# Kernel tuning notes

Hardware: AMD Instinct MI355X
Metric: run time of the kernel (lower is better)

## Reference

```python
import jax, jax.numpy as jnp
import numpy as np

B, S, E, H = 16, 2048, 512, 64


def setup_inputs() -> dict:
    key = jax.random.key(0)
    k1, k2, k3, k4, k5 = jax.random.split(key, 5)
    inp = {
        "input": jax.random.normal(k1, (B, S, E), dtype=jnp.float32),
        "seq_lengths": jax.random.randint(k2, (B,), 0, S).astype(jnp.int64),
        "Wq": jax.random.normal(k3, (E, H), dtype=jnp.float32) * (1.0 / np.sqrt(E)),
        "Wk": jax.random.normal(k4, (E, H), dtype=jnp.float32) * (1.0 / np.sqrt(E)),
        "Wv": jax.random.normal(k5, (E, H), dtype=jnp.float32) * (1.0 / np.sqrt(E)),
    }
    return inp


def reference(input, seq_lengths, Wq, Wk, Wv):
    # Projections (bias-free Linear): [B,S,E] @ [E,H] -> [B,S,H]
    q = input @ Wq
    k = input @ Wk
    v = input @ Wv
    Sdim = input.shape[1]
    head_size = Wk.shape[-1]
    # Padding mask: position >= seq_length -> True. Zero out q and k (NOT v),
    # exactly as the torch module does with masked_fill.
    pad = (jnp.arange(Sdim)[None, :] >= seq_lengths[:, None])[:, :, None]  # [B,S,1]
    q = jnp.where(pad, 0.0, q)
    k = jnp.where(pad, 0.0, k)
    scale = 1.0 / np.sqrt(head_size).astype(np.float32)
    # Full score matrix [B,S,S] (the memory-bound intermediate)
    scores = jnp.einsum("bsh,bth->bst", q, k) * scale
    weights = jax.nn.softmax(scores, axis=-1)
    weights = jnp.where(jnp.isnan(weights), 0.0, weights)
    out = jnp.einsum("bst,bth->bsh", weights, v)  # [B,S,H]
    return out
```

## Files before the change

kernel.cpp:

```cpp
#include <hip/hip_runtime.h>
#include <hip/hip_bf16.h>

typedef __bf16 bf16;
typedef __bf16 bf16x8 __attribute__((ext_vector_type(8)));
typedef __bf16 bf16x4 __attribute__((ext_vector_type(4)));
typedef float  f32x4  __attribute__((ext_vector_type(4)));

static constexpr int SDIM = 2048;
static constexpr int EDIM = 512;
static constexpr int HDIM = 64;

typedef __attribute__((address_space(1))) const void* gptr_t;
typedef __attribute__((address_space(3))) void*       lptr_t;

__device__ __forceinline__ void gl_lds16(const bf16* g, bf16* l) {
  __builtin_amdgcn_global_load_lds((gptr_t)g, (lptr_t)l, 16, 0, 0);
}

#if __has_builtin(__builtin_amdgcn_exp2f)
#define EXP2F(x) __builtin_amdgcn_exp2f(x)
#else
#define EXP2F(x) exp2f(x)
#endif

__device__ __forceinline__ bf16x8 pack8(f32x4 a, f32x4 b) {
  bf16x8 r;
  r[0] = (bf16)a[0]; r[1] = (bf16)a[1]; r[2] = (bf16)a[2]; r[3] = (bf16)a[3];
  r[4] = (bf16)b[0]; r[5] = (bf16)b[1]; r[6] = (bf16)b[2]; r[7] = (bf16)b[3];
  return r;
}

__global__ __launch_bounds__(256) void wt_kernel(const float* __restrict__ Wq,
                                                 const float* __restrict__ Wk,
                                                 const float* __restrict__ Wv,
                                                 bf16* __restrict__ Wt) {
  __shared__ float lds[64][65];
  const int mat = blockIdx.x >> 3;
  const int et  = blockIdx.x & 7;
  const float* W = (mat == 0) ? Wq : ((mat == 1) ? Wk : Wv);
  const float scale = (mat == 0) ? 0.18033688f : 1.0f;
  const int t  = threadIdx.x;
  const int er = t >> 2;
  const int c4 = (t & 3) * 16;
#pragma unroll
  for (int j = 0; j < 4; ++j) {
    f32x4 v = *(const f32x4*)(W + (size_t)(et * 64 + er) * HDIM + c4 + j * 4);
    lds[er][c4 + j * 4 + 0] = v[0]; lds[er][c4 + j * 4 + 1] = v[1];
    lds[er][c4 + j * 4 + 2] = v[2]; lds[er][c4 + j * 4 + 3] = v[3];
  }
  __syncthreads();
  const int h  = t >> 2;
  const int ec = (t & 3) * 16;
  bf16x8 o0, o1;
#pragma unroll
  for (int j = 0; j < 8; ++j) o0[j] = (bf16)(lds[ec + j][h] * scale);
#pragma unroll
  for (int j = 0; j < 8; ++j) o1[j] = (bf16)(lds[ec + 8 + j][h] * scale);
  bf16* dst = Wt + mat * (HDIM * EDIM) + (size_t)h * EDIM + et * 64 + ec;
  *(bf16x8*)dst = o0;
  *(bf16x8*)(dst + 8) = o1;
}

__global__ __launch_bounds__(256) void proj_kernel(const float* __restrict__ x,
                                                   const bf16* __restrict__ Wt,
                                                   const int* __restrict__ lens,
                                                   bf16* __restrict__ qo,
                                                   bf16* __restrict__ ko,
                                                   bf16* __restrict__ vT) {
  __shared__ __align__(16) bf16 wbuf[2][192 * 64];
  const int tid  = threadIdx.x;
  const int wave = tid >> 6;
  const int lane = tid & 63;
  const int quad = lane >> 4;
  const int l16  = lane & 15;
  const int rowbase = blockIdx.x * 64 + wave * 16;
  const int b = blockIdx.x >> 5;
  const float* xrow = x + (size_t)(rowbase + l16) * EDIM + quad * 8;
  const int srow   = lane >> 3;
  const int schunk = (lane & 7) ^ srow;

  #define WSTAGE(ck, buf) { _Pragma("unroll")                                  \
    for (int i6 = 0; i6 < 6; ++i6) {                                           \
      const int R0 = (wave * 6 + i6) * 8;                                      \
      gl_lds16(Wt + (size_t)(R0 + srow) * EDIM + (ck) * 64 + schunk * 8,       \
               &(buf)[R0 * 64]); } }

  f32x4 acc[3][4];
#pragma unroll
  for (int m = 0; m < 3; ++m)
#pragma unroll
    for (int nt = 0; nt < 4; ++nt) acc[m][nt] = (f32x4){0.f, 0.f, 0.f, 0.f};

  #define WCOMPUTE(buf, eo4, afrag) { _Pragma("unroll")                        \
    for (int m = 0; m < 3; ++m) { _Pragma("unroll")                            \
      for (int nt = 0; nt < 4; ++nt) {                                         \
        bf16x8 bfv = *(const bf16x8*)(&(buf)[(m * 64 + nt * 16 + l16) * 64 +   \
                                             ((((eo4) + quad) ^ (l16 & 7)) * 8)]); \
        acc[m][nt] = __builtin_amdgcn_mfma_f32_16x16x32_bf16(afrag, bfv, acc[m][nt], 0, 0, 0); } } }

  WSTAGE(0, wbuf[0]);
  f32x4 xA0 = *(const f32x4*)(xrow);
  f32x4 xB0 = *(const f32x4*)(xrow + 4);
  f32x4 xA1 = *(const f32x4*)(xrow + 32);
  f32x4 xB1 = *(const f32x4*)(xrow + 36);
#pragma unroll 2
  for (int ck = 0; ck < 8; ++ck) {
    __syncthreads();
    const int ksn = (ck < 7) ? (ck + 1) * 2 : 14;
    f32x4 nA0 = *(const f32x4*)(xrow + ksn * 32);
    f32x4 nB0 = *(const f32x4*)(xrow + ksn * 32 + 4);
    f32x4 nA1 = *(const f32x4*)(xrow + ksn * 32 + 32);
    f32x4 nB1 = *(const f32x4*)(xrow + ksn * 32 + 36);
    if (ck + 1 < 8) WSTAGE(ck + 1, wbuf[(ck + 1) & 1]);
    bf16x8 a = pack8(xA0, xB0);
    WCOMPUTE(wbuf[ck & 1], 0, a);
    a = pack8(xA1, xB1);
    WCOMPUTE(wbuf[ck & 1], 4, a);
    xA0 = nA0; xB0 = nB0; xA1 = nA1; xB1 = nB1;
  }

  int odd_or = 0;
#pragma unroll
  for (int i = 1; i < 16; i += 2) odd_or |= lens[i];
  const int len = (odd_or == 0) ? lens[2 * b] : lens[b];

#pragma unroll
  for (int nt = 0; nt < 4; ++nt) {
    const int h = nt * 16 + l16;
    bf16x4 vv;
#pragma unroll
    for (int r = 0; r < 4; ++r) {
      const int row = rowbase + quad * 4 + r;
      const int s = row & (SDIM - 1);
      const bool pad = (s >= len);
      qo[(size_t)row * HDIM + h] = (bf16)(pad ? 0.f : acc[0][nt][r]);
      ko[(size_t)row * HDIM + h] = (bf16)(pad ? 0.f : acc[1][nt][r]);
      vv[r] = (bf16)acc[2][nt][r];
    }
    *(bf16x4*)(vT + ((size_t)b * HDIM + h) * SDIM + (rowbase & (SDIM - 1)) + quad * 4) = vv;
  }
  #undef WSTAGE
  #undef WCOMPUTE
}

__global__ __launch_bounds__(256) void attn_kernel(const bf16* __restrict__ qb,
                                                   const bf16* __restrict__ kb,
                                                   const bf16* __restrict__ vT,
                                                   float* __restrict__ out) {
  __shared__ __align__(16) bf16 Kbuf[2][64 * 64];
  __shared__ __align__(16) bf16 Vbuf[2][64 * 64];
  __shared__ __align__(16) bf16 plds[4][2][16 * 64];
  const int tid  = threadIdx.x;
  const int wave = tid >> 6;
  const int lane = tid & 63;
  const int quad = lane >> 4;
  const int l16  = lane & 15;
  const int xcd = blockIdx.x & 7;
  const int jj  = blockIdx.x >> 3;
  const int b   = xcd * 2 + (jj >> 5);
  const int qbase = (jj & 31) * 64 + wave * 16;
  const bf16* q0 = qb + (size_t)b * SDIM * HDIM;
  const bf16* k0 = kb + (size_t)b * SDIM * HDIM;
  const bf16* v0 = vT + (size_t)b * HDIM * SDIM;
  const int swz = (l16 & 7) << 3;
  const int srow   = lane >> 3;
  const int schunk = (lane & 7) ^ (srow & 7);

  bf16x8 qf[2];
#pragma unroll
  for (int c = 0; c < 2; ++c)
    qf[c] = *(const bf16x8*)(q0 + (size_t)(qbase + l16) * HDIM + c * 32 + quad * 8);

  f32x4 O[4];
  float l_acc = 0.f;
#pragma unroll
  for (int ht = 0; ht < 4; ++ht) O[ht] = (f32x4){0.f, 0.f, 0.f, 0.f};
  bf16x8 vfp[4][2];

  #define STAGE(sidx, KB, VB)                                                  \
    {                                                                          \
      const int key0_ = (sidx) * 64;                                           \
      _Pragma("unroll")                                                        \
      for (int j8 = 0; j8 < 2; ++j8) {                                         \
        const int r0 = wave * 16 + j8 * 8;                                     \
        gl_lds16(k0 + (size_t)(key0_ + r0 + srow) * HDIM + schunk * 8,         \
                 &(KB)[r0 * 64]);                                              \
        gl_lds16(v0 + (size_t)(r0 + srow) * SDIM + key0_ + schunk * 8,         \
                 &(VB)[r0 * 64]);                                              \
      }                                                                        \
    }

  STAGE(0, Kbuf[0], Vbuf[0]);
#pragma unroll 2
  for (int s = 0; s < 32; ++s) {
    __syncthreads();
    if (s + 1 < 32) STAGE(s + 1, Kbuf[(s + 1) & 1], Vbuf[(s + 1) & 1]);
    const bf16* KB = Kbuf[s & 1];
    const bf16* VB = Vbuf[s & 1];
    bf16* PW = &plds[wave][s & 1][0];
    const bf16* PR = &plds[wave][(s & 1) ^ 1][0];

    bf16x8 pa[2];
    if (s) {
#pragma unroll
      for (int kc = 0; kc < 2; ++kc)
        pa[kc] = *(const bf16x8*)(&PR[l16 * 64 + (((kc * 4 + quad) << 3) ^ swz)]);
    }

    bf16x8 kf[4][2], vf[4][2];
#pragma unroll
    for (int kt = 0; kt < 4; ++kt)
#pragma unroll
      for (int c = 0; c < 2; ++c)
        kf[kt][c] = *(const bf16x8*)(&KB[(kt * 16 + l16) * 64 + (((c * 4 + quad) << 3) ^ swz)]);
#pragma unroll
    for (int ht = 0; ht < 4; ++ht)
#pragma unroll
      for (int kc = 0; kc < 2; ++kc)
        vf[ht][kc] = *(const bf16x8*)(&VB[(ht * 16 + l16) * 64 + (((kc * 4 + quad) << 3) ^ swz)]);

#pragma unroll
    for (int kt = 0; kt < 4; ++kt) {
      f32x4 st = (f32x4){0.f, 0.f, 0.f, 0.f};
      st = __builtin_amdgcn_mfma_f32_16x16x32_bf16(kf[kt][0], qf[0], st, 0, 0, 0);
      st = __builtin_amdgcn_mfma_f32_16x16x32_bf16(kf[kt][1], qf[1], st, 0, 0, 0);
      f32x4 p;
      p[0] = EXP2F(st[0]); p[1] = EXP2F(st[1]);
      p[2] = EXP2F(st[2]); p[3] = EXP2F(st[3]);
      l_acc += (p[0] + p[1]) + (p[2] + p[3]);
      bf16x4 pb;
      pb[0] = (bf16)p[0]; pb[1] = (bf16)p[1]; pb[2] = (bf16)p[2]; pb[3] = (bf16)p[3];
      const int coff = (((kt * 2 + (quad >> 1)) << 3) ^ swz) + (quad & 1) * 4;
      *(bf16x4*)(&PW[l16 * 64 + coff]) = pb;
    }

    if (s) {
#pragma unroll
      for (int ht = 0; ht < 4; ++ht) {
        O[ht] = __builtin_amdgcn_mfma_f32_16x16x32_bf16(pa[0], vfp[ht][0], O[ht], 0, 0, 0);
        O[ht] = __builtin_amdgcn_mfma_f32_16x16x32_bf16(pa[1], vfp[ht][1], O[ht], 0, 0, 0);
      }
    }
#pragma unroll
    for (int ht = 0; ht < 4; ++ht)
#pragma unroll
      for (int kc = 0; kc < 2; ++kc) vfp[ht][kc] = vf[ht][kc];
  }

  {
    bf16x8 pa[2];
    const bf16* PR = &plds[wave][1][0];
#pragma unroll
    for (int kc = 0; kc < 2; ++kc)
      pa[kc] = *(const bf16x8*)(&PR[l16 * 64 + (((kc * 4 + quad) << 3) ^ swz)]);
#pragma unroll
    for (int ht = 0; ht < 4; ++ht) {
      O[ht] = __builtin_amdgcn_mfma_f32_16x16x32_bf16(pa[0], vfp[ht][0], O[ht], 0, 0, 0);
      O[ht] = __builtin_amdgcn_mfma_f32_16x16x32_bf16(pa[1], vfp[ht][1], O[ht], 0, 0, 0);
    }
  }

  l_acc += __shfl_xor(l_acc, 16);
  l_acc += __shfl_xor(l_acc, 32);
  const float inv_own = 1.0f / l_acc;
#pragma unroll
  for (int r = 0; r < 4; ++r) {
    const float inv = __shfl(inv_own, (lane & 48) + quad * 4 + r);
    const int row = qbase + quad * 4 + r;
#pragma unroll
    for (int ht = 0; ht < 4; ++ht)
      out[((size_t)b * SDIM + row) * HDIM + ht * 16 + l16] = O[ht][r] * inv;
  }
  #undef STAGE
}

extern "C" void kernel_launch(void* const* d_in, const int* in_sizes, int n_in,
                              void* d_out, int out_size, void* d_ws, size_t ws_size,
                              hipStream_t stream) {
  (void)in_sizes; (void)n_in; (void)out_size; (void)ws_size;
  const float* x  = (const float*)d_in[0];
  const int*   sl = (const int*)d_in[1];
  const float* Wq = (const float*)d_in[2];
  const float* Wk = (const float*)d_in[3];
  const float* Wv = (const float*)d_in[4];
  float* out = (float*)d_out;

  char* ws = (char*)d_ws;
  bf16* Wt = (bf16*)(ws);
  bf16* qb = (bf16*)(ws + (256 << 10));
  bf16* kb = (bf16*)(ws + (256 << 10) + (4 << 20));
  bf16* vT = (bf16*)(ws + (256 << 10) + (8 << 20));

  wt_kernel  <<<24,  256, 0, stream>>>(Wq, Wk, Wv, Wt);
  proj_kernel<<<512, 256, 0, stream>>>(x, Wt, sl, qb, kb, vT);
  attn_kernel<<<512, 256, 0, stream>>>(qb, kb, vT, out);
}
```

Measured before the change: 140.4 us.

## Switch attention to 32x32 MFMA with register-resident P and split-K waves

The attention kernel moves from 16x16x32 to 32x32x16 bf16 MFMA tiles. Each pair of waves now takes 32 query rows and splits the key range in half, and the partial O and row sums are combined through LDS at the end. The P matrix is packed with v_cvt_pk_bf16 and rearranged with v_permlane32_swap so it stays in registers instead of going through an LDS round trip, and the one-step software pipeline of V fragments is dropped. This is meant to cut LDS traffic and improve MFMA efficiency, at the cost of an extra reduction phase and more registers per thread.

```diff
diff --git a/kernel.cpp b/kernel.cpp
--- a/kernel.cpp
+++ b/kernel.cpp
@@ -5,6 +5,8 @@
 typedef __bf16 bf16x8 __attribute__((ext_vector_type(8)));
 typedef __bf16 bf16x4 __attribute__((ext_vector_type(4)));
 typedef float  f32x4  __attribute__((ext_vector_type(4)));
+typedef float  f32x16 __attribute__((ext_vector_type(16)));
+typedef unsigned int u32x4 __attribute__((ext_vector_type(4)));
 
 static constexpr int SDIM = 2048;
 static constexpr int EDIM = 512;
@@ -27,6 +29,12 @@
   bf16x8 r;
   r[0] = (bf16)a[0]; r[1] = (bf16)a[1]; r[2] = (bf16)a[2]; r[3] = (bf16)a[3];
   r[4] = (bf16)b[0]; r[5] = (bf16)b[1]; r[6] = (bf16)b[2]; r[7] = (bf16)b[3];
+  return r;
+}
+
+__device__ __forceinline__ unsigned cvtpk_bf16(float a, float b) {
+  unsigned r;
+  asm("v_cvt_pk_bf16_f32 %0, %1, %2" : "=v"(r) : "v"(a), "v"(b));
   return r;
 }
 
@@ -147,129 +155,143 @@
                                                    const bf16* __restrict__ kb,
                                                    const bf16* __restrict__ vT,
                                                    float* __restrict__ out) {
-  __shared__ __align__(16) bf16 Kbuf[2][64 * 64];
-  __shared__ __align__(16) bf16 Vbuf[2][64 * 64];
-  __shared__ __align__(16) bf16 plds[4][2][16 * 64];
+  __shared__ __align__(16) bf16 Kbuf[2][2][64 * 64];
+  __shared__ __align__(16) bf16 Vbuf[2][2][64 * 64];
   const int tid  = threadIdx.x;
   const int wave = tid >> 6;
   const int lane = tid & 63;
-  const int quad = lane >> 4;
-  const int l16  = lane & 15;
+  const int hi   = lane >> 5;
+  const int l32  = lane & 31;
+  const int iq   = wave & 1;
+  const int jk   = wave >> 1;
   const int xcd = blockIdx.x & 7;
   const int jj  = blockIdx.x >> 3;
   const int b   = xcd * 2 + (jj >> 5);
-  const int qbase = (jj & 31) * 64 + wave * 16;
+  const int qbase = (jj & 31) * 64 + iq * 32;
   const bf16* q0 = qb + (size_t)b * SDIM * HDIM;
   const bf16* k0 = kb + (size_t)b * SDIM * HDIM;
   const bf16* v0 = vT + (size_t)b * HDIM * SDIM;
-  const int swz = (l16 & 7) << 3;
   const int srow   = lane >> 3;
-  const int schunk = (lane & 7) ^ (srow & 7);
-
-  bf16x8 qf[2];
-#pragma unroll
-  for (int c = 0; c < 2; ++c)
-    qf[c] = *(const bf16x8*)(q0 + (size_t)(qbase + l16) * HDIM + c * 32 + quad * 8);
-
-  f32x4 O[4];
+  const int schunk = (lane & 7) ^ srow;
+  const int rswz   = (l32 & 7) << 4;
+
+  bf16x8 qf[4];
+#pragma unroll
+  for (int c = 0; c < 4; ++c)
+    qf[c] = *(const bf16x8*)(q0 + (size_t)(qbase + l32) * HDIM + c * 16 + hi * 8);
+
+  f32x16 O[2];
+#pragma unroll
+  for (int ht = 0; ht < 2; ++ht)
+#pragma unroll
+    for (int r = 0; r < 16; ++r) O[ht][r] = 0.f;
   float l_acc = 0.f;
-#pragma unroll
-  for (int ht = 0; ht < 4; ++ht) O[ht] = (f32x4){0.f, 0.f, 0.f, 0.f};
-  bf16x8 vfp[4][2];
-
-  #define STAGE(sidx, KB, VB)                                                  \
-    {                                                                          \
-      const int key0_ = (sidx) * 64;                                           \
+
+  #define STAGE(sidx, db) {                                                    \
+    const int key0_ = (wave & 1) * 1024 + (sidx) * 64;                         \
+    if (wave < 2) {                                                            \
+      const bf16* gk = k0 + (size_t)(key0_ + srow) * HDIM + schunk * 8;        \
+      bf16* lk = &Kbuf[db][wave & 1][0];                                       \
       _Pragma("unroll")                                                        \
-      for (int j8 = 0; j8 < 2; ++j8) {                                         \
-        const int r0 = wave * 16 + j8 * 8;                                     \
-        gl_lds16(k0 + (size_t)(key0_ + r0 + srow) * HDIM + schunk * 8,         \
-                 &(KB)[r0 * 64]);                                              \
-        gl_lds16(v0 + (size_t)(r0 + srow) * SDIM + key0_ + schunk * 8,         \
-                 &(VB)[r0 * 64]);                                              \
-      }                                                                        \
+      for (int r8 = 0; r8 < 8; ++r8)                                           \
+        gl_lds16(gk + (size_t)r8 * 8 * HDIM, lk + r8 * 8 * 64);                \
+    } else {                                                                   \
+      const bf16* gv = v0 + (size_t)srow * SDIM + key0_ + schunk * 8;          \
+      bf16* lv = &Vbuf[db][wave & 1][0];                                       \
+      _Pragma("unroll")                                                        \
+      for (int r8 = 0; r8 < 8; ++r8)                                           \
+        gl_lds16(gv + (size_t)r8 * 8 * SDIM, lv + r8 * 8 * 64);                \
+    }                                                                          \
+  }
+
+  STAGE(0, 0);
+#pragma unroll 2
+  for (int s = 0; s < 16; ++s) {
+    __syncthreads();
+    if (s + 1 < 16) STAGE(s + 1, (s + 1) & 1);
+    const bf16* KB = &Kbuf[s & 1][jk][0];
+    const bf16* VB = &Vbuf[s & 1][jk][0];
+
+    bf16x8 pa[4];
+#pragma unroll
+    for (int kt = 0; kt < 2; ++kt) {
+      f32x16 st;
+#pragma unroll
+      for (int r = 0; r < 16; ++r) st[r] = 0.f;
+      const int krow = kt * 32 + l32;
+#pragma unroll
+      for (int c = 0; c < 4; ++c) {
+        bf16x8 kf = *(const bf16x8*)((const char*)KB + krow * 128 +
+                                     ((c * 32 + hi * 16) ^ rswz));
+        st = __builtin_amdgcn_mfma_f32_32x32x16_bf16(kf, qf[c], st, 0, 0, 0);
+      }
+      float p[16];
+#pragma unroll
+      for (int r = 0; r < 16; ++r) p[r] = EXP2F(st[r]);
+      float s0 = (p[0] + p[1]) + (p[2] + p[3]);
+      float s1 = (p[4] + p[5]) + (p[6] + p[7]);
+      float s2 = (p[8] + p[9]) + (p[10] + p[11]);
+      float s3 = (p[12] + p[13]) + (p[14] + p[15]);
+      l_acc += (s0 + s1) + (s2 + s3);
+      unsigned u0 = cvtpk_bf16(p[0], p[1]);
+      unsigned u1 = cvtpk_bf16(p[2], p[3]);
+      unsigned u2 = cvtpk_bf16(p[4], p[5]);
+      unsigned u3 = cvtpk_bf16(p[6], p[7]);
+      asm("v_permlane32_swap_b32 %0, %1" : "+v"(u0), "+v"(u2));
+      asm("v_permlane32_swap_b32 %0, %1" : "+v"(u1), "+v"(u3));
+      union { u32x4 u; bf16x8 v; } f0;
+      f0.u[0] = u0; f0.u[1] = u1; f0.u[2] = u2; f0.u[3] = u3;
+      pa[kt * 2 + 0] = f0.v;
+      unsigned u4 = cvtpk_bf16(p[8],  p[9]);
+      unsigned u5 = cvtpk_bf16(p[10], p[11]);
+      unsigned u6 = cvtpk_bf16(p[12], p[13]);
+      unsigned u7 = cvtpk_bf16(p[14], p[15]);
+      asm("v_permlane32_swap_b32 %0, %1" : "+v"(u4), "+v"(u6));
+      asm("v_permlane32_swap_b32 %0, %1" : "+v"(u5), "+v"(u7));
+      union { u32x4 u; bf16x8 v; } f1;
+      f1.u[0] = u4; f1.u[1] = u5; f1.u[2] = u6; f1.u[3] = u7;
+      pa[kt * 2 + 1] = f1.v;
     }
-
-  STAGE(0, Kbuf[0], Vbuf[0]);
-#pragma unroll 2
-  for (int s = 0; s < 32; ++s) {
-    __syncthreads();
-    if (s + 1 < 32) STAGE(s + 1, Kbuf[(s + 1) & 1], Vbuf[(s + 1) & 1]);
-    const bf16* KB = Kbuf[s & 1];
-    const bf16* VB = Vbuf[s & 1];
-    bf16* PW = &plds[wave][s & 1][0];
-    const bf16* PR = &plds[wave][(s & 1) ^ 1][0];
-
-    bf16x8 pa[2];
-    if (s) {
-#pragma unroll
-      for (int kc = 0; kc < 2; ++kc)
-        pa[kc] = *(const bf16x8*)(&PR[l16 * 64 + (((kc * 4 + quad) << 3) ^ swz)]);
-    }
-
-    bf16x8 kf[4][2], vf[4][2];
-#pragma unroll
-    for (int kt = 0; kt < 4; ++kt)
-#pragma unroll
-      for (int c = 0; c < 2; ++c)
-        kf[kt][c] = *(const bf16x8*)(&KB[(kt * 16 + l16) * 64 + (((c * 4 + quad) << 3) ^ swz)]);
-#pragma unroll
-    for (int ht = 0; ht < 4; ++ht)
-#pragma unroll
-      for (int kc = 0; kc < 2; ++kc)
-        vf[ht][kc] = *(const bf16x8*)(&VB[(ht * 16 + l16) * 64 + (((kc * 4 + quad) << 3) ^ swz)]);
-
-#pragma unroll
-    for (int kt = 0; kt < 4; ++kt) {
-      f32x4 st = (f32x4){0.f, 0.f, 0.f, 0.f};
-      st = __builtin_amdgcn_mfma_f32_16x16x32_bf16(kf[kt][0], qf[0], st, 0, 0, 0);
-      st = __builtin_amdgcn_mfma_f32_16x16x32_bf16(kf[kt][1], qf[1], st, 0, 0, 0);
-      f32x4 p;
-      p[0] = EXP2F(st[0]); p[1] = EXP2F(st[1]);
-      p[2] = EXP2F(st[2]); p[3] = EXP2F(st[3]);
-      l_acc += (p[0] + p[1]) + (p[2] + p[3]);
-      bf16x4 pb;
-      pb[0] = (bf16)p[0]; pb[1] = (bf16)p[1]; pb[2] = (bf16)p[2]; pb[3] = (bf16)p[3];
-      const int coff = (((kt * 2 + (quad >> 1)) << 3) ^ swz) + (quad & 1) * 4;
-      *(bf16x4*)(&PW[l16 * 64 + coff]) = pb;
-    }
-
-    if (s) {
-#pragma unroll
-      for (int ht = 0; ht < 4; ++ht) {
-        O[ht] = __builtin_amdgcn_mfma_f32_16x16x32_bf16(pa[0], vfp[ht][0], O[ht], 0, 0, 0);
-        O[ht] = __builtin_amdgcn_mfma_f32_16x16x32_bf16(pa[1], vfp[ht][1], O[ht], 0, 0, 0);
+#pragma unroll
+    for (int ht = 0; ht < 2; ++ht) {
+      const int vrow = ht * 32 + l32;
+#pragma unroll
+      for (int tc = 0; tc < 4; ++tc) {
+        bf16x8 vf = *(const bf16x8*)((const char*)VB + vrow * 128 +
+                                     ((tc * 32 + hi * 16) ^ rswz));
+        O[ht] = __builtin_amdgcn_mfma_f32_32x32x16_bf16(pa[tc], vf, O[ht], 0, 0, 0);
       }
     }
-#pragma unroll
-    for (int ht = 0; ht < 4; ++ht)
-#pragma unroll
-      for (int kc = 0; kc < 2; ++kc) vfp[ht][kc] = vf[ht][kc];
-  }
-
-  {
-    bf16x8 pa[2];
-    const bf16* PR = &plds[wave][1][0];
-#pragma unroll
-    for (int kc = 0; kc < 2; ++kc)
-      pa[kc] = *(const bf16x8*)(&PR[l16 * 64 + (((kc * 4 + quad) << 3) ^ swz)]);
-#pragma unroll
-    for (int ht = 0; ht < 4; ++ht) {
-      O[ht] = __builtin_amdgcn_mfma_f32_16x16x32_bf16(pa[0], vfp[ht][0], O[ht], 0, 0, 0);
-      O[ht] = __builtin_amdgcn_mfma_f32_16x16x32_bf16(pa[1], vfp[ht][1], O[ht], 0, 0, 0);
+  }
+
+  l_acc += __shfl_xor(l_acc, 32);
+
+  float* cb = (float*)&Kbuf[0][0][0];
+  float* cl = (float*)&Vbuf[0][0][0];
+  __syncthreads();
+  if (jk == 1) {
+#pragma unroll
+    for (int ht = 0; ht < 2; ++ht)
+#pragma unroll
+      for (int r = 0; r < 16; ++r) {
+        const int qrow = (r & 3) + 8 * (r >> 2) + 4 * hi;
+        cb[(iq * 32 + qrow) * 64 + ht * 32 + l32] = O[ht][r];
+      }
+    if (hi == 0) cl[iq * 32 + l32] = l_acc;
+  }
+  __syncthreads();
+  if (jk == 0) {
+    const float inv_own = 1.0f / (l_acc + cl[iq * 32 + l32]);
+#pragma unroll
+    for (int r = 0; r < 16; ++r) {
+      const int qrow = (r & 3) + 8 * (r >> 2) + 4 * hi;
+      const float inv = __shfl(inv_own, qrow);
+#pragma unroll
+      for (int ht = 0; ht < 2; ++ht) {
+        const float val = (O[ht][r] + cb[(iq * 32 + qrow) * 64 + ht * 32 + l32]) * inv;
+        out[((size_t)b * SDIM + qbase + qrow) * HDIM + ht * 32 + l32] = val;
+      }
     }
-  }
-
-  l_acc += __shfl_xor(l_acc, 16);
-  l_acc += __shfl_xor(l_acc, 32);
-  const float inv_own = 1.0f / l_acc;
-#pragma unroll
-  for (int r = 0; r < 4; ++r) {
-    const float inv = __shfl(inv_own, (lane & 48) + quad * 4 + r);
-    const int row = qbase + quad * 4 + r;
-#pragma unroll
-    for (int ht = 0; ht < 4; ++ht)
-      out[((size_t)b * SDIM + row) * HDIM + ht * 16 + l16] = O[ht][r] * inv;
   }
   #undef STAGE
 }
```

Result: faster. 136.9 us (-2.5%).
